# Kernel tuning notes

Hardware: AMD Instinct MI355X
Metric: run time of the kernel (lower is better)

The kernel has to match this reference:

```python
import jax, jax.numpy as jnp
import numpy as np

B, L, D, N = 4, 2048, 1024, 16


def setup_inputs() -> dict:
    key = jax.random.key(0)
    ks = jax.random.split(key, 12)
    s = 1.0 / np.sqrt(D)
    inp = {
        'x': jax.random.normal(ks[0], (B, L, D), jnp.float32),
        'ln_g': jnp.ones((D,), jnp.float32),
        'ln_b': jnp.zeros((D,), jnp.float32),
        'w1_w': jax.random.normal(ks[1], (D, D), jnp.float32) * s,
        'w1_b': jnp.zeros((D,), jnp.float32),
        'v1_w': jax.random.normal(ks[2], (D, D), jnp.float32) * s,
        'v1_b': jnp.zeros((D,), jnp.float32),
        'w2_w': jax.random.normal(ks[3], (D, D), jnp.float32) * s,
        'w2_b': jnp.zeros((D,), jnp.float32),
        'conv_w': jax.random.normal(ks[4], (D, 1, 3), jnp.float32) * (1.0 / np.sqrt(3.0)),
        'A_log': jnp.log(jnp.broadcast_to(jnp.arange(1, N + 1, dtype=jnp.float32), (D, N))),
        'D_skip': jnp.ones((D,), jnp.float32),
        'W_dt': jax.random.normal(ks[5], (D, D), jnp.float32) * (s * 0.1),
        'b_dt': jnp.full((D,), -4.0, jnp.float32),
        'W_B': jax.random.normal(ks[6], (D, N), jnp.float32) * s,
        'W_C': jax.random.normal(ks[7], (D, N), jnp.float32) * s,
    }
    return inp


def _layernorm(x, g, b, eps=1e-5):
    mu = jnp.mean(x, axis=-1, keepdims=True)
    var = jnp.mean(jnp.square(x - mu), axis=-1, keepdims=True)
    return (x - mu) * jax.lax.rsqrt(var + eps) * g + b


def _silu(x):
    return x * jax.nn.sigmoid(x)


def _depthwise_conv(x, w):
    # x: (B, L, D), w: (D, 1, 3), padding=1, groups=D
    xc = x.transpose(0, 2, 1)  # (B, D, L)
    y = jax.lax.conv_general_dilated(
        xc, w, window_strides=(1,), padding=[(1, 1)],
        feature_group_count=xc.shape[1],
        dimension_numbers=('NCH', 'OIH', 'NCH'))
    return y.transpose(0, 2, 1)


def _selective_scan(u, A_log, D_skip, W_dt, b_dt, W_B, W_C):
    # u: (B, L, D) -> y: (B, L, D); diagonal selective SSM (Mamba S6)
    A = -jnp.exp(A_log)                              # (D, N)
    dt = jax.nn.softplus(u @ W_dt + b_dt)            # (B, L, D)
    Bt = u @ W_B                                     # (B, L, N)
    Ct = u @ W_C                                     # (B, L, N)

    def step(h, inp):
        dt_t, B_t, C_t, u_t = inp                    # (B,D),(B,N),(B,N),(B,D)
        dA = jnp.exp(dt_t[..., None] * A)            # (B, D, N)
        h = dA * h + (dt_t * u_t)[..., None] * B_t[:, None, :]
        y = jnp.einsum('bdn,bn->bd', h, C_t)
        return h, y

    h0 = jnp.zeros((u.shape[0], u.shape[2], A.shape[1]), u.dtype)
    xs = (dt.transpose(1, 0, 2), Bt.transpose(1, 0, 2),
          Ct.transpose(1, 0, 2), u.transpose(1, 0, 2))
    _, ys = jax.lax.scan(step, h0, xs)               # ys: (L, B, D)
    return ys.transpose(1, 0, 2) + u * D_skip


def reference(x, ln_g, ln_b, w1_w, w1_b, v1_w, v1_b, w2_w, w2_b, conv_w,
              A_log, D_skip, W_dt, b_dt, W_B, W_C):
    x_norm = _layernorm(x, ln_g, ln_b)
    x1 = x_norm @ w1_w + w1_b
    x_conv = _silu(_depthwise_conv(x1, conv_w))
    x_ssm = _selective_scan(x_conv, A_log, D_skip, W_dt, b_dt, W_B, W_C)
    v = _silu(x_norm @ v1_w + v1_b)
    return (x_ssm * v) @ w2_w + w2_b
```

## Files before the change

### kernel.cpp

```cpp
#include <hip/hip_runtime.h>
#include <hip/hip_bf16.h>

#define BB 4
#define LL 2048
#define DD 1024
#define NN 16
#define BL (BB * LL)
#define NC 32
#define LC 64

typedef float f32x4 __attribute__((ext_vector_type(4)));
typedef __bf16 bf16x8 __attribute__((ext_vector_type(8)));

typedef __attribute__((address_space(1))) unsigned int as1_u32;
typedef __attribute__((address_space(3))) unsigned int as3_u32;

__device__ __forceinline__ void gl_lds16(const void* g, void* l) {
  __builtin_amdgcn_global_load_lds((as1_u32*)g, (as3_u32*)l, 16, 0, 0);
}

__device__ __forceinline__ float fast_sigmoid(float x) {
  return 1.f / (1.f + __expf(-x));
}

__global__ __launch_bounds__(256) void k_prep(const float* __restrict__ w1,
                                              const float* __restrict__ v1,
                                              const float* __restrict__ wdt,
                                              const float* __restrict__ w2,
                                              const float* __restrict__ WB,
                                              const float* __restrict__ WC,
                                              __hip_bfloat16* __restrict__ wcat,
                                              __hip_bfloat16* __restrict__ wdtbc,
                                              __hip_bfloat16* __restrict__ w2T) {
  const int z = blockIdx.z;
  if (z < 4) {
    const float* src = (z == 0) ? w1 : (z == 1) ? v1 : (z == 2) ? wdt : w2;
    __hip_bfloat16* dst = (z == 0) ? wcat
                        : (z == 1) ? (wcat + (size_t)1024 * DD)
                        : (z == 2) ? wdtbc : w2T;
    __shared__ float tile[32][33];
    const int kt = blockIdx.x * 32, nt = blockIdx.y * 32;
    const int tx = threadIdx.x & 31, ty = threadIdx.x >> 5;
#pragma unroll
    for (int j = 0; j < 32; j += 8)
      tile[ty + j][tx] = src[(size_t)(kt + ty + j) * DD + nt + tx];
    __syncthreads();
#pragma unroll
    for (int j = 0; j < 32; j += 8)
      dst[(size_t)(nt + ty + j) * DD + kt + tx] = __float2bfloat16(tile[tx][ty + j]);
  } else {
    const int id = blockIdx.y * 32 + blockIdx.x;
    if (id < 128) {
      const int idx = id * 256 + threadIdx.x;
      const int k = idx & 1023, n = idx >> 10;
      const float v = (n < 16) ? WB[(size_t)k * 16 + n] : WC[(size_t)k * 16 + (n - 16)];
      wdtbc[(size_t)(1024 + n) * DD + k] = __float2bfloat16(v);
    } else if (id < 512) {
      const int idx = (id - 128) * 256 + threadIdx.x;
      wdtbc[(size_t)1056 * DD + idx] = __float2bfloat16(0.f);
    }
  }
}

__global__ __launch_bounds__(256) void k_layernorm(const float* __restrict__ x,
                                                   const float* __restrict__ g,
                                                   const float* __restrict__ b,
                                                   __hip_bfloat16* __restrict__ out) {
  const int row = blockIdx.x;
  const int tid = threadIdx.x;
  const f32x4 xv = *(const f32x4*)(x + (size_t)row * DD + tid * 4);
  float s = xv[0] + xv[1] + xv[2] + xv[3];
  float sq = xv[0] * xv[0] + xv[1] * xv[1] + xv[2] * xv[2] + xv[3] * xv[3];
#pragma unroll
  for (int o = 32; o > 0; o >>= 1) {
    s += __shfl_down(s, o);
    sq += __shfl_down(sq, o);
  }
  __shared__ float red[8];
  const int wave = tid >> 6, lane = tid & 63;
  if (lane == 0) { red[wave] = s; red[4 + wave] = sq; }
  __syncthreads();
  s = red[0] + red[1] + red[2] + red[3];
  sq = red[4] + red[5] + red[6] + red[7];
  const float mean = s * (1.f / DD);
  const float var = sq * (1.f / DD) - mean * mean;
  const float rs = rsqrtf(var + 1e-5f);
  const f32x4 gv = *(const f32x4*)(g + tid * 4);
  const f32x4 bv = *(const f32x4*)(b + tid * 4);
  union { ushort4 u; __hip_bfloat16 h[4]; } cv;
#pragma unroll
  for (int j = 0; j < 4; ++j)
    cv.h[j] = __float2bfloat16((xv[j] - mean) * rs * gv[j] + bv[j]);
  *reinterpret_cast<ushort4*>(&out[(size_t)row * DD + tid * 4]) = cv.u;
}

template <int EPI>
__device__ __forceinline__ void gemm_body(const __hip_bfloat16* __restrict__ Ag,
                                          const __hip_bfloat16* __restrict__ Wg,
                                          void* __restrict__ o0, void* __restrict__ o1,
                                          void* __restrict__ o2,
                                          const float* __restrict__ bias0,
                                          const float* __restrict__ bias1) {
  __shared__ unsigned short As[2][128 * 32];
  __shared__ unsigned short Bs[2][128 * 32];
  const int tid = threadIdx.x;
  const int wave = tid >> 6, lane = tid & 63;
  const int quad = lane >> 4, l16 = lane & 15;
  const int wm = wave & 1, wn = wave >> 1;

  const int srow = wave * 32 + (lane >> 2);
  const int sbyte = (lane & 3) * 16;
  const char* gA = (const char*)(Ag + (size_t)(blockIdx.x * 128 + srow) * 1024) + sbyte;
  const char* gB = (const char*)(Wg + (size_t)(blockIdx.y * 128 + srow) * 1024) + sbyte;
  char* lA[2] = {(char*)&As[0][0] + wave * 2048, (char*)&As[1][0] + wave * 2048};
  char* lB[2] = {(char*)&Bs[0][0] + wave * 2048, (char*)&Bs[1][0] + wave * 2048};

  gl_lds16(gA, lA[0]);
  gl_lds16(gA + 16 * 2048, lA[0] + 1024);
  gl_lds16(gB, lB[0]);
  gl_lds16(gB + 16 * 2048, lB[0] + 1024);
  gA += 64;
  gB += 64;
  __syncthreads();

  f32x4 acc[4][4] = {};

  for (int kt = 0; kt < 32; ++kt) {
    const int cur = kt & 1, nxt = cur ^ 1;
    if (kt < 31) {
      gl_lds16(gA, lA[nxt]);
      gl_lds16(gA + 16 * 2048, lA[nxt] + 1024);
      gl_lds16(gB, lB[nxt]);
      gl_lds16(gB + 16 * 2048, lB[nxt] + 1024);
      gA += 64;
      gB += 64;
    }
    const unsigned short* Ab = &As[cur][0];
    const unsigned short* Bb = &Bs[cur][0];
    bf16x8 af[4], bfr[4];
#pragma unroll
    for (int i = 0; i < 4; ++i) {
      af[i] = *(const bf16x8*)(Ab + (wm * 64 + i * 16 + l16) * 32 + quad * 8);
      bfr[i] = *(const bf16x8*)(Bb + (wn * 64 + i * 16 + l16) * 32 + quad * 8);
    }
#pragma unroll
    for (int i = 0; i < 4; ++i)
#pragma unroll
      for (int j = 0; j < 4; ++j)
        acc[i][j] = __builtin_amdgcn_mfma_f32_16x16x32_bf16(af[i], bfr[j], acc[i][j], 0, 0, 0);
    __syncthreads();
  }

  const int m0 = blockIdx.x * 128 + wm * 64 + quad * 4;
  const int n0 = blockIdx.y * 128 + wn * 64 + l16;
#pragma unroll
  for (int i = 0; i < 4; ++i) {
#pragma unroll
    for (int r = 0; r < 4; ++r) {
      const int m = m0 + i * 16 + r;
#pragma unroll
      for (int j = 0; j < 4; ++j) {
        const int n = n0 + j * 16;
        const float val = acc[i][j][r];
        if constexpr (EPI == 1) {
          if (n < 1024) {
            ((__hip_bfloat16*)o0)[(size_t)m * DD + n] = __float2bfloat16(val + bias0[n]);
          } else {
            const float t = val + bias1[n - 1024];
            ((__hip_bfloat16*)o1)[(size_t)m * DD + (n - 1024)] =
                __float2bfloat16(t * fast_sigmoid(t));
          }
        } else if constexpr (EPI == 2) {
          if (n < 1024) {
            const float t = val + bias0[n];
            const float sp = (t > 15.f) ? t : __logf(1.f + __expf(t));
            ((__hip_bfloat16*)o0)[(size_t)m * DD + n] = __float2bfloat16(sp);
          } else if (n < 1040) {
            ((float*)o1)[(size_t)m * NN + (n - 1024)] = val;
          } else if (n < 1056) {
            ((float*)o2)[(size_t)m * NN + (n - 1040)] = val;
          }
        } else {
          ((float*)o0)[(size_t)m * DD + n] = val + bias0[n];
        }
      }
    }
  }
}

__global__ __launch_bounds__(256) void k_gemm_xv(const __hip_bfloat16* __restrict__ Ag,
                                                 const __hip_bfloat16* __restrict__ Wg,
                                                 void* o0, void* o1,
                                                 const float* __restrict__ b0,
                                                 const float* __restrict__ b1) {
  gemm_body<1>(Ag, Wg, o0, o1, nullptr, b0, b1);
}
__global__ __launch_bounds__(256) void k_gemm_dbc(const __hip_bfloat16* __restrict__ Ag,
                                                  const __hip_bfloat16* __restrict__ Wg,
                                                  void* o0, void* o1, void* o2,
                                                  const float* __restrict__ b0) {
  gemm_body<2>(Ag, Wg, o0, o1, o2, b0, nullptr);
}
__global__ __launch_bounds__(256) void k_gemm_out(const __hip_bfloat16* __restrict__ Ag,
                                                  const __hip_bfloat16* __restrict__ Wg,
                                                  void* o0, const float* __restrict__ b0) {
  gemm_body<3>(Ag, Wg, o0, nullptr, nullptr, b0, nullptr);
}

__global__ __launch_bounds__(256) void k_conv_silu(const __hip_bfloat16* __restrict__ x1,
                                                   const float* __restrict__ w,
                                                   __hip_bfloat16* __restrict__ out) {
  const size_t e = ((size_t)blockIdx.x * 256 + threadIdx.x) * 8;
  const int d = (int)(e & 1023);
  const int l = (int)((e >> 10) & 2047);
  const bf16x8 zero = {};
  const bf16x8 xm = (l > 0) ? *(const bf16x8*)(x1 + e - DD) : zero;
  const bf16x8 x0 = *(const bf16x8*)(x1 + e);
  const bf16x8 xp = (l < LL - 1) ? *(const bf16x8*)(x1 + e + DD) : zero;
  bf16x8 o;
#pragma unroll
  for (int j = 0; j < 8; ++j) {
    const float w0 = w[(d + j) * 3 + 0], w1 = w[(d + j) * 3 + 1], w2 = w[(d + j) * 3 + 2];
    const float a = w0 * (float)xm[j] + w1 * (float)x0[j] + w2 * (float)xp[j];
    o[j] = (__bf16)(a * fast_sigmoid(a));
  }
  *(bf16x8*)(out + e) = o;
}

__global__ __launch_bounds__(256) void k_scan1(const __hip_bfloat16* __restrict__ dt,
                                               const __hip_bfloat16* __restrict__ u,
                                               const float* __restrict__ Bt,
                                               const float* __restrict__ A_log,
                                               float* __restrict__ P,
                                               float* __restrict__ hend) {
  const int d = blockIdx.x * 256 + threadIdx.x;
  const int c = blockIdx.y, b = blockIdx.z;
  __shared__ float Bsh[LC * NN];
  ((f32x4*)Bsh)[threadIdx.x] = ((const f32x4*)(Bt + (size_t)(b * LL + c * LC) * NN))[threadIdx.x];
  float a[NN];
#pragma unroll
  for (int n = 0; n < NN; ++n) a[n] = -__expf(A_log[(size_t)d * NN + n]);
  __syncthreads();
  float h[NN] = {};
  float sdt = 0.f;
  size_t idx = (size_t)(b * LL + c * LC) * DD + d;
#pragma unroll 4
  for (int t = 0; t < LC; ++t, idx += DD) {
    const float dtv = __bfloat162float(dt[idx]);
    const float uv = __bfloat162float(u[idx]);
    sdt += dtv;
    const float du = dtv * uv;
#pragma unroll
    for (int n = 0; n < NN; ++n)
      h[n] = __expf(dtv * a[n]) * h[n] + du * Bsh[t * NN + n];
  }
  const size_t o = ((size_t)((b * NC + c) * DD + d)) * NN;
#pragma unroll
  for (int n = 0; n < NN; ++n) {
    P[o + n] = __expf(sdt * a[n]);
    hend[o + n] = h[n];
  }
}

__global__ __launch_bounds__(256) void k_scan2(const float* __restrict__ P, float* __restrict__ h) {
  const int gidx = blockIdx.x * 256 + threadIdx.x;
  const int n = gidx & 15, d = (gidx >> 4) & 1023, b = gidx >> 14;
  float hs = 0.f;
  size_t off = ((size_t)b * NC * DD + d) * NN + n;
  const size_t stride = (size_t)DD * NN;
  for (int c = 0; c < NC; ++c, off += stride) {
    const float he = h[off];
    const float p = P[off];
    h[off] = hs;
    hs = p * hs + he;
  }
}

__global__ __launch_bounds__(256) void k_scan3(const __hip_bfloat16* __restrict__ dt,
                                               const __hip_bfloat16* __restrict__ u,
                                               const float* __restrict__ Bt,
                                               const float* __restrict__ Ct,
                                               const float* __restrict__ A_log,
                                               const float* __restrict__ hstart,
                                               const float* __restrict__ Dskip,
                                               const __hip_bfloat16* __restrict__ v,
                                               __hip_bfloat16* __restrict__ yA) {
  const int d = blockIdx.x * 256 + threadIdx.x;
  const int c = blockIdx.y, b = blockIdx.z;
  __shared__ float Bsh[LC * NN];
  __shared__ float Csh[LC * NN];
  ((f32x4*)Bsh)[threadIdx.x] = ((const f32x4*)(Bt + (size_t)(b * LL + c * LC) * NN))[threadIdx.x];
  ((f32x4*)Csh)[threadIdx.x] = ((const f32x4*)(Ct + (size_t)(b * LL + c * LC) * NN))[threadIdx.x];
  float a[NN];
#pragma unroll
  for (int n = 0; n < NN; ++n) a[n] = -__expf(A_log[(size_t)d * NN + n]);
  const float dsk = Dskip[d];
  float h[NN];
  const size_t o = ((size_t)((b * NC + c) * DD + d)) * NN;
#pragma unroll
  for (int n = 0; n < NN; ++n) h[n] = hstart[o + n];
  __syncthreads();
  size_t idx = (size_t)(b * LL + c * LC) * DD + d;
#pragma unroll 2
  for (int t = 0; t < LC; ++t, idx += DD) {
    const float dtv = __bfloat162float(dt[idx]);
    const float uv = __bfloat162float(u[idx]);
    const float du = dtv * uv;
    float y = 0.f;
#pragma unroll
    for (int n = 0; n < NN; ++n) {
      h[n] = __expf(dtv * a[n]) * h[n] + du * Bsh[t * NN + n];
      y += h[n] * Csh[t * NN + n];
    }
    const float xssm = y + uv * dsk;
    const float vv = __bfloat162float(v[idx]);
    yA[idx] = __float2bfloat16(xssm * vv);
  }
}

extern "C" void kernel_launch(void* const* d_in, const int* in_sizes, int n_in,
                              void* d_out, int out_size, void* d_ws, size_t ws_size,
                              hipStream_t stream) {
  const float* x      = (const float*)d_in[0];
  const float* ln_g   = (const float*)d_in[1];
  const float* ln_b   = (const float*)d_in[2];
  const float* w1_w   = (const float*)d_in[3];
  const float* w1_b   = (const float*)d_in[4];
  const float* v1_w   = (const float*)d_in[5];
  const float* v1_b   = (const float*)d_in[6];
  const float* w2_w   = (const float*)d_in[7];
  const float* w2_b   = (const float*)d_in[8];
  const float* conv_w = (const float*)d_in[9];
  const float* A_log  = (const float*)d_in[10];
  const float* D_skip = (const float*)d_in[11];
  const float* W_dt   = (const float*)d_in[12];
  const float* b_dt   = (const float*)d_in[13];
  const float* W_B    = (const float*)d_in[14];
  const float* W_C    = (const float*)d_in[15];

  char* ws = (char*)d_ws;
  const size_t OFF_SLOTA = 0;
  const size_t OFF_SLOTB = 16777216;
  const size_t OFF_VBUF  = 33554432;
  const size_t OFF_YA    = 50331648;
  const size_t OFF_WCAT  = 67108864;
  const size_t OFF_WDTBC = 71303168;
  const size_t OFF_W2T   = 73662464;
  const size_t OFF_BT    = 75759616;
  const size_t OFF_CT    = 76283904;
  const size_t OFF_P     = 76808192;
  const size_t OFF_H     = 85196800;

  __hip_bfloat16* xnorm = (__hip_bfloat16*)(ws + OFF_SLOTA);
  __hip_bfloat16* xconv = (__hip_bfloat16*)(ws + OFF_SLOTA);
  __hip_bfloat16* x1    = (__hip_bfloat16*)(ws + OFF_SLOTB);
  __hip_bfloat16* dtb   = (__hip_bfloat16*)(ws + OFF_SLOTB);
  __hip_bfloat16* vbuf  = (__hip_bfloat16*)(ws + OFF_VBUF);
  __hip_bfloat16* yA    = (__hip_bfloat16*)(ws + OFF_YA);
  __hip_bfloat16* wcat  = (__hip_bfloat16*)(ws + OFF_WCAT);
  __hip_bfloat16* wdtbc = (__hip_bfloat16*)(ws + OFF_WDTBC);
  __hip_bfloat16* w2T   = (__hip_bfloat16*)(ws + OFF_W2T);
  float* Btf = (float*)(ws + OFF_BT);
  float* Ctf = (float*)(ws + OFF_CT);
  float* P   = (float*)(ws + OFF_P);
  float* H   = (float*)(ws + OFF_H);

  k_prep<<<dim3(32, 32, 5), 256, 0, stream>>>(w1_w, v1_w, W_dt, w2_w, W_B, W_C,
                                              wcat, wdtbc, w2T);

  k_layernorm<<<BL, 256, 0, stream>>>(x, ln_g, ln_b, xnorm);

  k_gemm_xv<<<dim3(BL / 128, 2048 / 128), 256, 0, stream>>>(
      xnorm, wcat, (void*)x1, (void*)vbuf, w1_b, v1_b);

  k_conv_silu<<<(BL * DD / 8) / 256, 256, 0, stream>>>(x1, conv_w, xconv);

  k_gemm_dbc<<<dim3(BL / 128, 1152 / 128), 256, 0, stream>>>(
      xconv, wdtbc, (void*)dtb, (void*)Btf, (void*)Ctf, b_dt);

  k_scan1<<<dim3(DD / 256, NC, BB), 256, 0, stream>>>(dtb, xconv, Btf, A_log, P, H);
  k_scan2<<<(BB * DD * NN) / 256, 256, 0, stream>>>(P, H);
  k_scan3<<<dim3(DD / 256, NC, BB), 256, 0, stream>>>(dtb, xconv, Btf, Ctf, A_log, H, D_skip,
                                                      vbuf, yA);

  k_gemm_out<<<dim3(BL / 128, 1024 / 128), 256, 0, stream>>>(yA, w2T, d_out, w2_b);
}
```

Baseline: 375.3 us.

## Widen GEMM tiles to 128x256, drop double buffering, fuse layernorm into prep

The GEMM tile grows from 128x128 to 128x256, so each wave holds 4x8 accumulators and every A load is reused across twice as many columns. The LDS double buffering is removed: loads are now issued, synchronised and consumed within each k-step, so load latency is no longer hidden behind the MFMAs. The layernorm kernel is folded into the weight-prep kernel as extra z-slices, saving one launch. The wdtbc padding is extended to 1280 rows to fit the wider tile. Fewer blocks and higher register pressure may reduce occupancy and overlap.

```diff
diff --git a/kernel.cpp b/kernel.cpp
--- a/kernel.cpp
+++ b/kernel.cpp
@@ -8,6 +8,7 @@
 #define BL (BB * LL)
 #define NC 32
 #define LC 64
+#define MB 1048576
 
 typedef float f32x4 __attribute__((ext_vector_type(4)));
 typedef __bf16 bf16x8 __attribute__((ext_vector_type(8)));
@@ -23,22 +24,27 @@
   return 1.f / (1.f + __expf(-x));
 }
 
-__global__ __launch_bounds__(256) void k_prep(const float* __restrict__ w1,
-                                              const float* __restrict__ v1,
-                                              const float* __restrict__ wdt,
-                                              const float* __restrict__ w2,
-                                              const float* __restrict__ WB,
-                                              const float* __restrict__ WC,
-                                              __hip_bfloat16* __restrict__ wcat,
-                                              __hip_bfloat16* __restrict__ wdtbc,
-                                              __hip_bfloat16* __restrict__ w2T) {
+__global__ __launch_bounds__(256) void k_prep_ln(const float* __restrict__ w1,
+                                                 const float* __restrict__ v1,
+                                                 const float* __restrict__ wdt,
+                                                 const float* __restrict__ w2,
+                                                 const float* __restrict__ WB,
+                                                 const float* __restrict__ WC,
+                                                 __hip_bfloat16* __restrict__ wcat,
+                                                 __hip_bfloat16* __restrict__ wdtbc,
+                                                 __hip_bfloat16* __restrict__ w2T,
+                                                 const float* __restrict__ x,
+                                                 const float* __restrict__ ln_g,
+                                                 const float* __restrict__ ln_b,
+                                                 __hip_bfloat16* __restrict__ xnorm) {
   const int z = blockIdx.z;
+  __shared__ float tile[32][33];
+  __shared__ float red[8];
   if (z < 4) {
     const float* src = (z == 0) ? w1 : (z == 1) ? v1 : (z == 2) ? wdt : w2;
     __hip_bfloat16* dst = (z == 0) ? wcat
                         : (z == 1) ? (wcat + (size_t)1024 * DD)
                         : (z == 2) ? wdtbc : w2T;
-    __shared__ float tile[32][33];
     const int kt = blockIdx.x * 32, nt = blockIdx.y * 32;
     const int tx = threadIdx.x & 31, ty = threadIdx.x >> 5;
 #pragma unroll
@@ -48,50 +54,44 @@
 #pragma unroll
     for (int j = 0; j < 32; j += 8)
       dst[(size_t)(nt + ty + j) * DD + kt + tx] = __float2bfloat16(tile[tx][ty + j]);
-  } else {
+  } else if (z == 4) {
     const int id = blockIdx.y * 32 + blockIdx.x;
     if (id < 128) {
       const int idx = id * 256 + threadIdx.x;
       const int k = idx & 1023, n = idx >> 10;
       const float v = (n < 16) ? WB[(size_t)k * 16 + n] : WC[(size_t)k * 16 + (n - 16)];
       wdtbc[(size_t)(1024 + n) * DD + k] = __float2bfloat16(v);
-    } else if (id < 512) {
+    } else {
       const int idx = (id - 128) * 256 + threadIdx.x;
       wdtbc[(size_t)1056 * DD + idx] = __float2bfloat16(0.f);
     }
-  }
-}
-
-__global__ __launch_bounds__(256) void k_layernorm(const float* __restrict__ x,
-                                                   const float* __restrict__ g,
-                                                   const float* __restrict__ b,
-                                                   __hip_bfloat16* __restrict__ out) {
-  const int row = blockIdx.x;
-  const int tid = threadIdx.x;
-  const f32x4 xv = *(const f32x4*)(x + (size_t)row * DD + tid * 4);
-  float s = xv[0] + xv[1] + xv[2] + xv[3];
-  float sq = xv[0] * xv[0] + xv[1] * xv[1] + xv[2] * xv[2] + xv[3] * xv[3];
-#pragma unroll
-  for (int o = 32; o > 0; o >>= 1) {
-    s += __shfl_down(s, o);
-    sq += __shfl_down(sq, o);
-  }
-  __shared__ float red[8];
-  const int wave = tid >> 6, lane = tid & 63;
-  if (lane == 0) { red[wave] = s; red[4 + wave] = sq; }
-  __syncthreads();
-  s = red[0] + red[1] + red[2] + red[3];
-  sq = red[4] + red[5] + red[6] + red[7];
-  const float mean = s * (1.f / DD);
-  const float var = sq * (1.f / DD) - mean * mean;
-  const float rs = rsqrtf(var + 1e-5f);
-  const f32x4 gv = *(const f32x4*)(g + tid * 4);
-  const f32x4 bv = *(const f32x4*)(b + tid * 4);
-  union { ushort4 u; __hip_bfloat16 h[4]; } cv;
-#pragma unroll
-  for (int j = 0; j < 4; ++j)
-    cv.h[j] = __float2bfloat16((xv[j] - mean) * rs * gv[j] + bv[j]);
-  *reinterpret_cast<ushort4*>(&out[(size_t)row * DD + tid * 4]) = cv.u;
+  } else {
+    const int row = (z - 5) * 1024 + blockIdx.y * 32 + blockIdx.x;
+    const int tid = threadIdx.x;
+    const f32x4 xv = *(const f32x4*)(x + (size_t)row * DD + tid * 4);
+    float s = xv[0] + xv[1] + xv[2] + xv[3];
+    float sq = xv[0] * xv[0] + xv[1] * xv[1] + xv[2] * xv[2] + xv[3] * xv[3];
+#pragma unroll
+    for (int o = 32; o > 0; o >>= 1) {
+      s += __shfl_down(s, o);
+      sq += __shfl_down(sq, o);
+    }
+    const int wave = tid >> 6, lane = tid & 63;
+    if (lane == 0) { red[wave] = s; red[4 + wave] = sq; }
+    __syncthreads();
+    s = red[0] + red[1] + red[2] + red[3];
+    sq = red[4] + red[5] + red[6] + red[7];
+    const float mean = s * (1.f / DD);
+    const float var = sq * (1.f / DD) - mean * mean;
+    const float rs = rsqrtf(var + 1e-5f);
+    const f32x4 gv = *(const f32x4*)(ln_g + tid * 4);
+    const f32x4 bv = *(const f32x4*)(ln_b + tid * 4);
+    union { ushort4 u; __hip_bfloat16 h[4]; } cv;
+#pragma unroll
+    for (int j = 0; j < 4; ++j)
+      cv.h[j] = __float2bfloat16((xv[j] - mean) * rs * gv[j] + bv[j]);
+    *reinterpret_cast<ushort4*>(&xnorm[(size_t)row * DD + tid * 4]) = cv.u;
+  }
 }
 
 template <int EPI>
@@ -101,66 +101,58 @@
                                           void* __restrict__ o2,
                                           const float* __restrict__ bias0,
                                           const float* __restrict__ bias1) {
-  __shared__ unsigned short As[2][128 * 32];
-  __shared__ unsigned short Bs[2][128 * 32];
+  __shared__ unsigned short As[128 * 32];
+  __shared__ unsigned short Bs[256 * 32];
   const int tid = threadIdx.x;
   const int wave = tid >> 6, lane = tid & 63;
   const int quad = lane >> 4, l16 = lane & 15;
   const int wm = wave & 1, wn = wave >> 1;
 
-  const int srow = wave * 32 + (lane >> 2);
+  const int srowA = wave * 32 + (lane >> 2);
+  const int srowB = wave * 64 + (lane >> 2);
   const int sbyte = (lane & 3) * 16;
-  const char* gA = (const char*)(Ag + (size_t)(blockIdx.x * 128 + srow) * 1024) + sbyte;
-  const char* gB = (const char*)(Wg + (size_t)(blockIdx.y * 128 + srow) * 1024) + sbyte;
-  char* lA[2] = {(char*)&As[0][0] + wave * 2048, (char*)&As[1][0] + wave * 2048};
-  char* lB[2] = {(char*)&Bs[0][0] + wave * 2048, (char*)&Bs[1][0] + wave * 2048};
-
-  gl_lds16(gA, lA[0]);
-  gl_lds16(gA + 16 * 2048, lA[0] + 1024);
-  gl_lds16(gB, lB[0]);
-  gl_lds16(gB + 16 * 2048, lB[0] + 1024);
-  gA += 64;
-  gB += 64;
-  __syncthreads();
-
-  f32x4 acc[4][4] = {};
+  const char* gA = (const char*)(Ag + (size_t)(blockIdx.x * 128 + srowA) * 1024) + sbyte;
+  const char* gB = (const char*)(Wg + (size_t)(blockIdx.y * 256 + srowB) * 1024) + sbyte;
+  char* lA = (char*)As + wave * 2048;
+  char* lB = (char*)Bs + wave * 4096;
+
+  f32x4 acc[4][8] = {};
 
   for (int kt = 0; kt < 32; ++kt) {
-    const int cur = kt & 1, nxt = cur ^ 1;
-    if (kt < 31) {
-      gl_lds16(gA, lA[nxt]);
-      gl_lds16(gA + 16 * 2048, lA[nxt] + 1024);
-      gl_lds16(gB, lB[nxt]);
-      gl_lds16(gB + 16 * 2048, lB[nxt] + 1024);
-      gA += 64;
-      gB += 64;
-    }
-    const unsigned short* Ab = &As[cur][0];
-    const unsigned short* Bb = &Bs[cur][0];
-    bf16x8 af[4], bfr[4];
-#pragma unroll
-    for (int i = 0; i < 4; ++i) {
-      af[i] = *(const bf16x8*)(Ab + (wm * 64 + i * 16 + l16) * 32 + quad * 8);
-      bfr[i] = *(const bf16x8*)(Bb + (wn * 64 + i * 16 + l16) * 32 + quad * 8);
-    }
+    gl_lds16(gA, lA);
+    gl_lds16(gA + 16 * 2048, lA + 1024);
+    gl_lds16(gB, lB);
+    gl_lds16(gB + 16 * 2048, lB + 1024);
+    gl_lds16(gB + 32 * 2048, lB + 2048);
+    gl_lds16(gB + 48 * 2048, lB + 3072);
+    gA += 64;
+    gB += 64;
+    __syncthreads();
+    bf16x8 af[4], bfr[8];
 #pragma unroll
     for (int i = 0; i < 4; ++i)
-#pragma unroll
-      for (int j = 0; j < 4; ++j)
+      af[i] = *(const bf16x8*)(As + (wm * 64 + i * 16 + l16) * 32 + quad * 8);
+#pragma unroll
+    for (int j = 0; j < 8; ++j)
+      bfr[j] = *(const bf16x8*)(Bs + (wn * 128 + j * 16 + l16) * 32 + quad * 8);
+#pragma unroll
+    for (int i = 0; i < 4; ++i)
+#pragma unroll
+      for (int j = 0; j < 8; ++j)
         acc[i][j] = __builtin_amdgcn_mfma_f32_16x16x32_bf16(af[i], bfr[j], acc[i][j], 0, 0, 0);
     __syncthreads();
   }
 
-  const int m0 = blockIdx.x * 128 + wm * 64 + quad * 4;
-  const int n0 = blockIdx.y * 128 + wn * 64 + l16;
+  const int em0 = blockIdx.x * 128 + wm * 64 + quad * 4;
+  const int en0 = blockIdx.y * 256 + wn * 128 + l16;
 #pragma unroll
   for (int i = 0; i < 4; ++i) {
 #pragma unroll
     for (int r = 0; r < 4; ++r) {
-      const int m = m0 + i * 16 + r;
-#pragma unroll
-      for (int j = 0; j < 4; ++j) {
-        const int n = n0 + j * 16;
+      const int m = em0 + i * 16 + r;
+#pragma unroll
+      for (int j = 0; j < 8; ++j) {
+        const int n = en0 + j * 16;
         const float val = acc[i][j][r];
         if constexpr (EPI == 1) {
           if (n < 1024) {
@@ -340,16 +332,16 @@
 
   char* ws = (char*)d_ws;
   const size_t OFF_SLOTA = 0;
-  const size_t OFF_SLOTB = 16777216;
-  const size_t OFF_VBUF  = 33554432;
-  const size_t OFF_YA    = 50331648;
-  const size_t OFF_WCAT  = 67108864;
-  const size_t OFF_WDTBC = 71303168;
-  const size_t OFF_W2T   = 73662464;
-  const size_t OFF_BT    = 75759616;
-  const size_t OFF_CT    = 76283904;
-  const size_t OFF_P     = 76808192;
-  const size_t OFF_H     = 85196800;
+  const size_t OFF_SLOTB = (size_t)16 * MB;
+  const size_t OFF_VBUF  = (size_t)32 * MB;
+  const size_t OFF_YA    = (size_t)48 * MB;
+  const size_t OFF_WCAT  = (size_t)64 * MB;
+  const size_t OFF_WDTBC = (size_t)68 * MB;
+  const size_t OFF_W2T   = OFF_WDTBC + 2621440;
+  const size_t OFF_BT    = OFF_W2T + 2097152;
+  const size_t OFF_CT    = OFF_BT + 524288;
+  const size_t OFF_P     = OFF_CT + 524288;
+  const size_t OFF_H     = OFF_P + 8388608;
 
   __hip_bfloat16* xnorm = (__hip_bfloat16*)(ws + OFF_SLOTA);
   __hip_bfloat16* xconv = (__hip_bfloat16*)(ws + OFF_SLOTA);
@@ -365,17 +357,15 @@
   float* P   = (float*)(ws + OFF_P);
   float* H   = (float*)(ws + OFF_H);
 
-  k_prep<<<dim3(32, 32, 5), 256, 0, stream>>>(w1_w, v1_w, W_dt, w2_w, W_B, W_C,
-                                              wcat, wdtbc, w2T);
-
-  k_layernorm<<<BL, 256, 0, stream>>>(x, ln_g, ln_b, xnorm);
-
-  k_gemm_xv<<<dim3(BL / 128, 2048 / 128), 256, 0, stream>>>(
+  k_prep_ln<<<dim3(32, 32, 13), 256, 0, stream>>>(w1_w, v1_w, W_dt, w2_w, W_B, W_C,
+                                                  wcat, wdtbc, w2T, x, ln_g, ln_b, xnorm);
+
+  k_gemm_xv<<<dim3(BL / 128, 2048 / 256), 256, 0, stream>>>(
       xnorm, wcat, (void*)x1, (void*)vbuf, w1_b, v1_b);
 
   k_conv_silu<<<(BL * DD / 8) / 256, 256, 0, stream>>>(x1, conv_w, xconv);
 
-  k_gemm_dbc<<<dim3(BL / 128, 1152 / 128), 256, 0, stream>>>(
+  k_gemm_dbc<<<dim3(BL / 128, 1280 / 256), 256, 0, stream>>>(
       xconv, wdtbc, (void*)dtb, (void*)Btf, (void*)Ctf, b_dt);
 
   k_scan1<<<dim3(DD / 256, NC, BB), 256, 0, stream>>>(dtb, xconv, Btf, A_log, P, H);
@@ -383,5 +373,5 @@
   k_scan3<<<dim3(DD / 256, NC, BB), 256, 0, stream>>>(dtb, xconv, Btf, Ctf, A_log, H, D_skip,
                                                       vbuf, yA);
 
-  k_gemm_out<<<dim3(BL / 128, 1024 / 128), 256, 0, stream>>>(yA, w2T, d_out, w2_b);
-}
+  k_gemm_out<<<dim3(BL / 128, 1024 / 256), 256, 0, stream>>>(yA, w2T, d_out, w2_b);
+}
```

New measurement: 499.3 us. 1.33x slower.
